# Kernel tuning notes

Hardware: AMD Instinct MI355X
Metric: run time of the kernel (lower is better)

The kernel has to match this reference:

```python
import jax, jax.numpy as jnp
import numpy as np

N_NODES = 50000
N_EDGES = 500000
D = 256  # node_dim = edge_dim = out_dim; in_dim = 2*D


def setup_inputs() -> dict:
    key = jax.random.key(0)
    ks = jax.random.split(key, 9)
    x = jax.random.normal(ks[0], (N_NODES, D), dtype=jnp.float32)
    edge_index = jax.random.randint(ks[1], (2, N_EDGES), 0, N_NODES, dtype=jnp.int64)
    edge_attr = jax.random.normal(ks[2], (N_EDGES, D), dtype=jnp.float32)
    u = jax.random.normal(ks[3], (1, D), dtype=jnp.float32)
    batch = jnp.zeros((N_NODES,), dtype=jnp.int64)
    scale = 1.0 / np.sqrt(2 * D)
    W1 = jax.random.normal(ks[4], (2 * D, D), dtype=jnp.float32) * scale
    b1 = jax.random.normal(ks[5], (D,), dtype=jnp.float32) * scale
    W2 = jax.random.normal(ks[6], (2 * D, D), dtype=jnp.float32) * scale
    b2 = jax.random.normal(ks[7], (D,), dtype=jnp.float32) * scale
    return {"x": x, "edge_index": edge_index, "edge_attr": edge_attr, "u": u,
            "batch": batch, "W1": W1, "b1": b1, "W2": W2, "b2": b2}


def reference(x, edge_index, edge_attr, u, batch, W1, b1, W2, b2):
    row, col = edge_index[0], edge_index[1]
    # gather source-node features and concat with edge features: [E, 2D]
    h = jnp.concatenate([x[row], edge_attr], axis=1)
    h = jax.nn.relu(h @ W1 + b1)  # node_mlp_1
    # scatter-mean over destination nodes
    agg = jax.ops.segment_sum(h, col, num_segments=N_NODES)
    cnt = jax.ops.segment_sum(jnp.ones((h.shape[0],), h.dtype), col, num_segments=N_NODES)
    agg = agg / jnp.maximum(cnt, 1.0)[:, None]
    out = jnp.concatenate([x, agg], axis=1)  # [N, 2D]
    return jax.nn.relu(out @ W2 + b2)  # node_mlp_2
```

## Files before the change

kernel.cpp:

```cpp
#include <hip/hip_runtime.h>

#define N_NODES 50000
#define N_EDGES 500000
#define D 256
#define TWO_D 512

typedef __attribute__((ext_vector_type(8))) __bf16 bf16x8;
typedef __attribute__((ext_vector_type(4))) float f32x4;
typedef unsigned short ushort_t;

__device__ __forceinline__ unsigned short f2bf(float f) {
    unsigned int u = __builtin_bit_cast(unsigned int, f);
    u += 0x7FFFu + ((u >> 16) & 1u);
    return (unsigned short)(u >> 16);
}
__device__ __forceinline__ unsigned int pk2(float lo, float hi) {
    return (unsigned int)f2bf(lo) | ((unsigned int)f2bf(hi) << 16);
}


__global__ void k_zero(float* __restrict__ p, int n4) {
    int i = blockIdx.x * blockDim.x + threadIdx.x;
    if (i < n4) ((float4*)p)[i] = make_float4(0.f, 0.f, 0.f, 0.f);
}

__global__ void k_cvt_x(const float* __restrict__ x, ushort_t* __restrict__ xb, int n8) {
    int i = blockIdx.x * blockDim.x + threadIdx.x;
    if (i < n8) {
        const float4* s = (const float4*)(x + (size_t)i * 8);
        float4 a = s[0], b = s[1];
        uint4 o;
        o.x = pk2(a.x, a.y); o.y = pk2(a.z, a.w);
        o.z = pk2(b.x, b.y); o.w = pk2(b.z, b.w);
        *(uint4*)(xb + (size_t)i * 8) = o;
    }
}

__global__ void k_wt(const float* __restrict__ w, ushort_t* __restrict__ wt, int KW) {
    int n = blockIdx.x;
    for (int k = threadIdx.x; k < KW; k += blockDim.x)
        wt[(size_t)n * KW + k] = f2bf(w[(size_t)k * D + n]);
}

__global__ void k_count_i(const int* __restrict__ coli, int* __restrict__ cnt) {
    int e = blockIdx.x * blockDim.x + threadIdx.x;
    if (e < N_EDGES) atomicAdd(&cnt[coli[e]], 1);
}


__device__ __forceinline__ int iscan_block(int v, int tid) {
    int lane = tid & 63, wv = tid >> 6;
    int s = v;
    #pragma unroll
    for (int off = 1; off < 64; off <<= 1) {
        int t = __shfl_up(s, off, 64);
        if (lane >= off) s += t;
    }
    __shared__ int wsum[4];
    if (lane == 63) wsum[wv] = s;
    __syncthreads();
    #pragma unroll
    for (int w = 0; w < 3; ++w)
        if (wv > w) s += wsum[w];
    return s;
}

__global__ void k_scan_a(const int* __restrict__ cnt, int* __restrict__ rowptr,
                         int* __restrict__ bsum) {
    int i = blockIdx.x * 256 + threadIdx.x;
    int v = (i < N_NODES) ? cnt[i] : 0;
    int s = iscan_block(v, threadIdx.x);
    if (i < N_NODES) rowptr[i] = s - v;
    if (threadIdx.x == 255) bsum[blockIdx.x] = s;
}

__global__ void k_scan_b(int* __restrict__ bsum, int nb) {
    int i = threadIdx.x;
    int v = (i < nb) ? bsum[i] : 0;
    int s = iscan_block(v, i);
    if (i < nb) bsum[i] = s - v;
}

__global__ void k_scan_c(int* __restrict__ rowptr, const int* __restrict__ bsum,
                         int* __restrict__ cursor) {
    int i = blockIdx.x * 256 + threadIdx.x;
    if (i < N_NODES) {
        int r = rowptr[i] + bsum[blockIdx.x];
        rowptr[i] = r;
        cursor[i] = r;
    }
    if (i == 0) rowptr[N_NODES] = N_EDGES;
}

__global__ void k_fill(const int* __restrict__ coli, const int* __restrict__ rowi,
                       int* __restrict__ cursor, int* __restrict__ elist,
                       int* __restrict__ rowg) {
    int e = blockIdx.x * blockDim.x + threadIdx.x;
    if (e < N_EDGES) {
        int p = atomicAdd(&cursor[coli[e]], 1);
        elist[p] = e;
        rowg[p] = rowi[e];
    }
}

__global__ void k_posnode(const int* __restrict__ rowptr, int* __restrict__ posnode) {
    int p = blockIdx.x * blockDim.x + threadIdx.x;
    if (p >= N_EDGES) return;
    int lo = 0, hi = N_NODES;
    while (hi - lo > 1) {
        int mid = (lo + hi) >> 1;
        if (rowptr[mid] <= p) lo = mid; else hi = mid;
    }
    posnode[p] = lo;
}

__global__ __launch_bounds__(256) void k_xw1(
    const ushort_t* __restrict__ xb, const ushort_t* __restrict__ w1at,
    const float* __restrict__ b1, float* __restrict__ xw1)
{
    __shared__ __align__(16) ushort_t As[64 * 64];
    __shared__ __align__(16) ushort_t Bs[256 * 64];
    const int tid = threadIdx.x;
    const int wave = tid >> 6, lane = tid & 63;
    const int lr = lane & 15, lh = lane >> 4;
    const int n0 = blockIdx.x * 64;

    const int sm = tid >> 2;
    const int sc = (tid & 3) << 4;
    int ns = n0 + sm; if (ns >= N_NODES) ns = N_NODES - 1;
    const ushort_t* xrow = xb + (size_t)ns * D;
    const ushort_t* wrow = w1at + (size_t)tid * D;
    const int swA = (sm & 7) << 3;
    const int swB = (tid & 7) << 3;

    f32x4 acc[4][4];
    #pragma unroll
    for (int i = 0; i < 4; ++i)
        #pragma unroll
        for (int j = 0; j < 4; ++j)
            acc[i][j] = (f32x4){0.f, 0.f, 0.f, 0.f};

    for (int kk = 0; kk < 4; ++kk) {
        const int k0 = kk << 6;
        const uint4* sx = (const uint4*)(xrow + k0 + sc);
        uint4 av0 = sx[0], av1 = sx[1];
        const uint4* wsv = (const uint4*)(wrow + k0);
        uint4 w0 = wsv[0], w1 = wsv[1], w2 = wsv[2], w3 = wsv[3];
        uint4 w4 = wsv[4], w5 = wsv[5], w6 = wsv[6], w7 = wsv[7];

        __syncthreads();
        *(uint4*)&As[sm * 64 + ( sc      ^ swA)] = av0;
        *(uint4*)&As[sm * 64 + ((sc + 8) ^ swA)] = av1;
        {
            const int base = tid * 64;
            *(uint4*)&Bs[base + ( 0 ^ swB)] = w0;
            *(uint4*)&Bs[base + ( 8 ^ swB)] = w1;
            *(uint4*)&Bs[base + (16 ^ swB)] = w2;
            *(uint4*)&Bs[base + (24 ^ swB)] = w3;
            *(uint4*)&Bs[base + (32 ^ swB)] = w4;
            *(uint4*)&Bs[base + (40 ^ swB)] = w5;
            *(uint4*)&Bs[base + (48 ^ swB)] = w6;
            *(uint4*)&Bs[base + (56 ^ swB)] = w7;
        }
        __syncthreads();

        #pragma unroll
        for (int kh = 0; kh < 2; ++kh) {
            const int kb = kh * 32 + lh * 8;
            bf16x8 af[4], bfr[4];
            #pragma unroll
            for (int i = 0; i < 4; ++i) {
                int m = i * 16 + lr;
                af[i] = *(const bf16x8*)&As[m * 64 + (kb ^ ((m & 7) << 3))];
            }
            #pragma unroll
            for (int j = 0; j < 4; ++j) {
                int n = wave * 64 + j * 16 + lr;
                bfr[j] = *(const bf16x8*)&Bs[n * 64 + (kb ^ ((n & 7) << 3))];
            }
            #pragma unroll
            for (int i = 0; i < 4; ++i)
                #pragma unroll
                for (int j = 0; j < 4; ++j)
                    acc[i][j] = __builtin_amdgcn_mfma_f32_16x16x32_bf16(af[i], bfr[j], acc[i][j], 0, 0, 0);
        }
    }

    float bv[4];
    #pragma unroll
    for (int j = 0; j < 4; ++j) bv[j] = b1[wave * 64 + j * 16 + lr];
    #pragma unroll
    for (int i = 0; i < 4; ++i) {
        #pragma unroll
        for (int r = 0; r < 4; ++r) {
            int m = i * 16 + lh * 4 + r;
            int node = n0 + m;
            if (node < N_NODES) {
                float* orow = xw1 + (size_t)node * D;
                #pragma unroll
                for (int j = 0; j < 4; ++j)
                    orow[wave * 64 + j * 16 + lr] = acc[i][j][r] + bv[j];
            }
        }
    }
}

__global__ __launch_bounds__(256, 3) void k_edge_csr(
    const float* __restrict__ ea, const ushort_t* __restrict__ w1bt,
    const float* __restrict__ xw1, const int* __restrict__ elist,
    const int* __restrict__ rowg, const int* __restrict__ posnode,
    const int* __restrict__ rowptr, float* __restrict__ agg)
{
    __shared__ __align__(16) ushort_t As[64 * 40];
    __shared__ __align__(16) ushort_t Bs[256 * 40];
    __shared__ int snd[64];
    const int tid = threadIdx.x;
    const int wave = tid >> 6, lane = tid & 63;
    const int lr = lane & 15, lh = lane >> 4;
    const int p0 = blockIdx.x * 64;

    if (tid < 64) {
        int p = p0 + tid;
        snd[tid] = (p < N_EDGES) ? posnode[min(p, N_EDGES - 1)] : -1;
    }

    const int sm = tid >> 2;
    const int scq = (tid & 3) << 3;
    int ps = p0 + sm; if (ps >= N_EDGES) ps = N_EDGES - 1;
    const int es = elist[ps];
    const float* earow = ea + (size_t)es * D;
    const ushort_t* wrow = w1bt + (size_t)tid * D;

    f32x4 acc[4][4];
    #pragma unroll
    for (int i = 0; i < 4; ++i)
        #pragma unroll
        for (int j = 0; j < 4; ++j)
            acc[i][j] = (f32x4){0.f, 0.f, 0.f, 0.f};

    #pragma unroll 1
    for (int kk = 0; kk < 8; ++kk) {
        const int k0 = kk << 5;
        const float4* s = (const float4*)(earow + k0 + scq);
        float4 f0 = s[0], f1 = s[1];
        uint4 av;
        av.x = pk2(f0.x, f0.y); av.y = pk2(f0.z, f0.w);
        av.z = pk2(f1.x, f1.y); av.w = pk2(f1.z, f1.w);
        const uint4* w = (const uint4*)(wrow + k0);
        uint4 w0 = w[0], w1 = w[1], w2 = w[2], w3 = w[3];

        __syncthreads();
        *(uint4*)&As[sm * 40 + scq] = av;
        {
            ushort_t* bb = &Bs[tid * 40];
            *(uint4*)&bb[ 0] = w0;
            *(uint4*)&bb[ 8] = w1;
            *(uint4*)&bb[16] = w2;
            *(uint4*)&bb[24] = w3;
        }
        __syncthreads();

        {
            const int kb = lh * 8;
            bf16x8 af[4], bfr[4];
            #pragma unroll
            for (int i = 0; i < 4; ++i)
                af[i] = *(const bf16x8*)&As[(i * 16 + lr) * 40 + kb];
            #pragma unroll
            for (int j = 0; j < 4; ++j)
                bfr[j] = *(const bf16x8*)&Bs[(wave * 64 + j * 16 + lr) * 40 + kb];
            #pragma unroll
            for (int i = 0; i < 4; ++i)
                #pragma unroll
                for (int j = 0; j < 4; ++j)
                    acc[i][j] = __builtin_amdgcn_mfma_f32_16x16x32_bf16(af[i], bfr[j], acc[i][j], 0, 0, 0);
        }
    }

    #pragma unroll
    for (int i = 0; i < 4; ++i) {
        #pragma unroll
        for (int r = 0; r < 4; ++r) {
            const int m = i * 16 + lh * 4 + r;
            const bool ok = (p0 + m < N_EDGES);
            const int srw = rowg[min(p0 + m, N_EDGES - 1)];
            const float* xr = xw1 + (size_t)srw * D + wave * 64 + lr;
            #pragma unroll
            for (int j = 0; j < 4; ++j) {
                float v = acc[i][j][r] + xr[j * 16];
                v = v > 0.f ? v : 0.f;
                acc[i][j][r] = ok ? v : 0.f;
            }
        }
    }

    int a = 0;
    while (a < 64) {
        const int node = snd[a];
        int b = a + 1;
        while (b < 64 && snd[b] == node) ++b;
        if (node >= 0) {
            float s0 = 0.f, s1 = 0.f, s2 = 0.f, s3 = 0.f;
            #pragma unroll
            for (int i = 0; i < 4; ++i) {
                if (b <= i * 16 || a >= (i + 1) * 16) continue;
                #pragma unroll
                for (int r = 0; r < 4; ++r) {
                    const int m = i * 16 + lh * 4 + r;
                    const bool in = (m >= a) && (m < b);
                    s0 += in ? acc[i][0][r] : 0.f;
                    s1 += in ? acc[i][1][r] : 0.f;
                    s2 += in ? acc[i][2][r] : 0.f;
                    s3 += in ? acc[i][3][r] : 0.f;
                }
            }
            s0 += __shfl_xor(s0, 16, 64); s0 += __shfl_xor(s0, 32, 64);
            s1 += __shfl_xor(s1, 16, 64); s1 += __shfl_xor(s1, 32, 64);
            s2 += __shfl_xor(s2, 16, 64); s2 += __shfl_xor(s2, 32, 64);
            s3 += __shfl_xor(s3, 16, 64); s3 += __shfl_xor(s3, 32, 64);
            if (lh == 0) {
                const bool interior = (rowptr[node] >= p0) && (rowptr[node + 1] <= p0 + 64);
                float* dst = agg + (size_t)node * D + wave * 64 + lr;
                if (interior) {
                    dst[0]  = s0; dst[16] = s1; dst[32] = s2; dst[48] = s3;
                } else {
                    atomicAdd(&dst[0],  s0); atomicAdd(&dst[16], s1);
                    atomicAdd(&dst[32], s2); atomicAdd(&dst[48], s3);
                }
            }
        }
        a = b;
    }
}

__global__ __launch_bounds__(256) void k_node(
    const ushort_t* __restrict__ xb, const float* __restrict__ agg,
    const int* __restrict__ cnti,
    const ushort_t* __restrict__ w2t, const float* __restrict__ b2,
    float* __restrict__ out)
{
    __shared__ __align__(16) ushort_t As[64 * 64];
    __shared__ __align__(16) ushort_t Bs[256 * 64];
    const int tid = threadIdx.x;
    const int wave = tid >> 6, lane = tid & 63;
    const int lr = lane & 15, lh = lane >> 4;
    const int n0 = blockIdx.x * 64;

    const int sm = tid >> 2;
    const int sc = (tid & 3) << 4;
    int ns = n0 + sm; if (ns >= N_NODES) ns = N_NODES - 1;
    const ushort_t* xrow = xb + (size_t)ns * D;
    const float*    arow = agg + (size_t)ns * D;
    const float     ic   = 1.0f / fmaxf((float)cnti[ns], 1.0f);
    const ushort_t* wrow = w2t + (size_t)tid * TWO_D;
    const int swA = (sm & 7) << 3;
    const int swB = (tid & 7) << 3;

    f32x4 acc[4][4];
    #pragma unroll
    for (int i = 0; i < 4; ++i)
        #pragma unroll
        for (int j = 0; j < 4; ++j)
            acc[i][j] = (f32x4){0.f, 0.f, 0.f, 0.f};

    for (int kk = 0; kk < 8; ++kk) {
        const int k0 = kk << 6;
        uint4 av0, av1;
        if (kk < 4) {
            const uint4* s = (const uint4*)(xrow + k0 + sc);
            av0 = s[0]; av1 = s[1];
        } else {
            const float4* s = (const float4*)(arow + (k0 - D) + sc);
            float4 f0 = s[0], f1 = s[1], f2 = s[2], f3 = s[3];
            f0.x *= ic; f0.y *= ic; f0.z *= ic; f0.w *= ic;
            f1.x *= ic; f1.y *= ic; f1.z *= ic; f1.w *= ic;
            f2.x *= ic; f2.y *= ic; f2.z *= ic; f2.w *= ic;
            f3.x *= ic; f3.y *= ic; f3.z *= ic; f3.w *= ic;
            av0.x = pk2(f0.x, f0.y); av0.y = pk2(f0.z, f0.w);
            av0.z = pk2(f1.x, f1.y); av0.w = pk2(f1.z, f1.w);
            av1.x = pk2(f2.x, f2.y); av1.y = pk2(f2.z, f2.w);
            av1.z = pk2(f3.x, f3.y); av1.w = pk2(f3.z, f3.w);
        }
        const uint4* wsv = (const uint4*)(wrow + k0);
        uint4 w0 = wsv[0], w1 = wsv[1], w2 = wsv[2], w3 = wsv[3];
        uint4 w4 = wsv[4], w5 = wsv[5], w6 = wsv[6], w7 = wsv[7];

        __syncthreads();
        *(uint4*)&As[sm * 64 + ( sc      ^ swA)] = av0;
        *(uint4*)&As[sm * 64 + ((sc + 8) ^ swA)] = av1;
        {
            const int base = tid * 64;
            *(uint4*)&Bs[base + ( 0 ^ swB)] = w0;
            *(uint4*)&Bs[base + ( 8 ^ swB)] = w1;
            *(uint4*)&Bs[base + (16 ^ swB)] = w2;
            *(uint4*)&Bs[base + (24 ^ swB)] = w3;
            *(uint4*)&Bs[base + (32 ^ swB)] = w4;
            *(uint4*)&Bs[base + (40 ^ swB)] = w5;
            *(uint4*)&Bs[base + (48 ^ swB)] = w6;
            *(uint4*)&Bs[base + (56 ^ swB)] = w7;
        }
        __syncthreads();

        #pragma unroll
        for (int kh = 0; kh < 2; ++kh) {
            const int kb = kh * 32 + lh * 8;
            bf16x8 af[4], bfr[4];
            #pragma unroll
            for (int i = 0; i < 4; ++i) {
                int m = i * 16 + lr;
                af[i] = *(const bf16x8*)&As[m * 64 + (kb ^ ((m & 7) << 3))];
            }
            #pragma unroll
            for (int j = 0; j < 4; ++j) {
                int n = wave * 64 + j * 16 + lr;
                bfr[j] = *(const bf16x8*)&Bs[n * 64 + (kb ^ ((n & 7) << 3))];
            }
            #pragma unroll
            for (int i = 0; i < 4; ++i)
                #pragma unroll
                for (int j = 0; j < 4; ++j)
                    acc[i][j] = __builtin_amdgcn_mfma_f32_16x16x32_bf16(af[i], bfr[j], acc[i][j], 0, 0, 0);
        }
    }

    float bv[4];
    #pragma unroll
    for (int j = 0; j < 4; ++j) bv[j] = b2[wave * 64 + j * 16 + lr];
    #pragma unroll
    for (int i = 0; i < 4; ++i) {
        #pragma unroll
        for (int r = 0; r < 4; ++r) {
            int m = i * 16 + lh * 4 + r;
            int node = n0 + m;
            if (node < N_NODES) {
                float* orow = out + (size_t)node * D;
                #pragma unroll
                for (int j = 0; j < 4; ++j) {
                    float v = acc[i][j][r] + bv[j];
                    orow[wave * 64 + j * 16 + lr] = v > 0.f ? v : 0.f;
                }
            }
        }
    }
}


extern "C" void kernel_launch(void* const* d_in, const int* in_sizes, int n_in,
                              void* d_out, int out_size, void* d_ws, size_t ws_size,
                              hipStream_t stream)
{
    const float* x  = (const float*)d_in[0];
    const int*   ei = (const int*)d_in[1];
    const float* ea = (const float*)d_in[2];
    const float* W1 = (const float*)d_in[5];
    const float* b1 = (const float*)d_in[6];
    const float* W2 = (const float*)d_in[7];
    const float* b2 = (const float*)d_in[8];
    float* out = (float*)d_out;

    const int* rowi = ei;
    const int* coli = ei + N_EDGES;
    char* ws = (char*)d_ws;

    size_t off = 0;
    auto take = [&](size_t bytes) {
        char* p = ws + off;
        off = (off + bytes + 255) & ~(size_t)255;
        return p;
    };

    ushort_t* xb      = (ushort_t*)take((size_t)N_NODES * D * 2);
    ushort_t* w1at    = (ushort_t*)take((size_t)D * D * 2);
    ushort_t* w1bt    = (ushort_t*)take((size_t)D * D * 2);
    ushort_t* w2t     = (ushort_t*)take((size_t)D * TWO_D * 2);
    float*    xw1     = (float*)take((size_t)N_NODES * D * 4);
    float*    agg     = (float*)take((size_t)N_NODES * D * 4);
    int*      cnti    = (int*)take(50016 * 4);
    int*      rowptr  = (int*)take(50016 * 4);
    int*      cursor  = (int*)take(50016 * 4);
    int*      bsum    = (int*)take(256 * 4);
    int*      elist   = (int*)take((size_t)N_EDGES * 4);
    int*      rowg    = (int*)take((size_t)N_EDGES * 4);
    int*      posnode = (int*)take((size_t)N_EDGES * 4);

    const int NB = (N_NODES + 255) / 256;
    const int EB = (N_EDGES + 255) / 256;
    const int NGB = (N_NODES + 63) / 64;
    const int EGB = (N_EDGES + 63) / 64;

    k_cvt_x<<<(N_NODES * D / 8 + 255) / 256, 256, 0, stream>>>(x, xb, N_NODES * D / 8);
    k_wt   <<<D, 256, 0, stream>>>(W1, w1at, D);
    k_wt   <<<D, 256, 0, stream>>>(W1 + (size_t)D * D, w1bt, D);
    k_wt   <<<D, 256, 0, stream>>>(W2, w2t, TWO_D);

    k_zero   <<<49, 256, 0, stream>>>((float*)cnti, 50016 / 4);
    k_count_i<<<EB, 256, 0, stream>>>(coli, cnti);
    k_scan_a <<<NB, 256, 0, stream>>>(cnti, rowptr, bsum);
    k_scan_b <<<1, 256, 0, stream>>>(bsum, NB);
    k_scan_c <<<NB, 256, 0, stream>>>(rowptr, bsum, cursor);
    k_fill   <<<EB, 256, 0, stream>>>(coli, rowi, cursor, elist, rowg);
    k_posnode<<<EB, 256, 0, stream>>>(rowptr, posnode);

    k_xw1    <<<NGB, 256, 0, stream>>>(xb, w1at, b1, xw1);
    k_zero   <<<(N_NODES * D / 4 + 255) / 256, 256, 0, stream>>>(agg, N_NODES * D / 4);
    k_edge_csr<<<EGB, 256, 0, stream>>>(ea, w1bt, xw1, elist, rowg, posnode, rowptr, agg);
    k_node   <<<NGB, 256, 0, stream>>>(xb, agg, cnti, w2t, b2, out);
}
```

Measured before the change: 502.4 us.

## Load MFMA operands directly from global memory, dropping LDS staging in edge kernel

The edge GEMM kernel no longer stages the edge-feature and weight tiles through shared memory with two barriers per K step. Each lane now loads its own A fragments (converted from fp32 to bf16) and B fragments straight from global memory into registers, and the K loop is unrolled by two. This removes the LDS traffic and the synchronisation, but each of the four waves now loads the full A tile separately, so A-side global and cache traffic is four times higher. The per-lane accesses are also less coalesced. A barrier is added before the segment reduction so the shared node-index array is ready.

```diff
diff --git a/kernel.cpp b/kernel.cpp
--- a/kernel.cpp
+++ b/kernel.cpp
@@ -211,8 +211,6 @@
     const int* __restrict__ rowg, const int* __restrict__ posnode,
     const int* __restrict__ rowptr, float* __restrict__ agg)
 {
-    __shared__ __align__(16) ushort_t As[64 * 40];
-    __shared__ __align__(16) ushort_t Bs[256 * 40];
     __shared__ int snd[64];
     const int tid = threadIdx.x;
     const int wave = tid >> 6, lane = tid & 63;
@@ -224,12 +222,16 @@
         snd[tid] = (p < N_EDGES) ? posnode[min(p, N_EDGES - 1)] : -1;
     }
 
-    const int sm = tid >> 2;
-    const int scq = (tid & 3) << 3;
-    int ps = p0 + sm; if (ps >= N_EDGES) ps = N_EDGES - 1;
-    const int es = elist[ps];
-    const float* earow = ea + (size_t)es * D;
-    const ushort_t* wrow = w1bt + (size_t)tid * D;
+    const float* pea[4];
+    #pragma unroll
+    for (int i = 0; i < 4; ++i) {
+        const int p = min(p0 + i * 16 + lr, N_EDGES - 1);
+        pea[i] = ea + (size_t)elist[p] * D + lh * 8;
+    }
+    const ushort_t* pw[4];
+    #pragma unroll
+    for (int j = 0; j < 4; ++j)
+        pw[j] = w1bt + (size_t)(wave * 64 + j * 16 + lr) * D + lh * 8;
 
     f32x4 acc[4][4];
     #pragma unroll
@@ -238,43 +240,27 @@
         for (int j = 0; j < 4; ++j)
             acc[i][j] = (f32x4){0.f, 0.f, 0.f, 0.f};
 
-    #pragma unroll 1
+    #pragma unroll 2
     for (int kk = 0; kk < 8; ++kk) {
         const int k0 = kk << 5;
-        const float4* s = (const float4*)(earow + k0 + scq);
-        float4 f0 = s[0], f1 = s[1];
-        uint4 av;
-        av.x = pk2(f0.x, f0.y); av.y = pk2(f0.z, f0.w);
-        av.z = pk2(f1.x, f1.y); av.w = pk2(f1.z, f1.w);
-        const uint4* w = (const uint4*)(wrow + k0);
-        uint4 w0 = w[0], w1 = w[1], w2 = w[2], w3 = w[3];
-
-        __syncthreads();
-        *(uint4*)&As[sm * 40 + scq] = av;
-        {
-            ushort_t* bb = &Bs[tid * 40];
-            *(uint4*)&bb[ 0] = w0;
-            *(uint4*)&bb[ 8] = w1;
-            *(uint4*)&bb[16] = w2;
-            *(uint4*)&bb[24] = w3;
-        }
-        __syncthreads();
-
-        {
-            const int kb = lh * 8;
-            bf16x8 af[4], bfr[4];
-            #pragma unroll
-            for (int i = 0; i < 4; ++i)
-                af[i] = *(const bf16x8*)&As[(i * 16 + lr) * 40 + kb];
+        bf16x8 af[4], bfr[4];
+        #pragma unroll
+        for (int i = 0; i < 4; ++i) {
+            const float4* s = (const float4*)(pea[i] + k0);
+            float4 f0 = s[0], f1 = s[1];
+            uint4 av;
+            av.x = pk2(f0.x, f0.y); av.y = pk2(f0.z, f0.w);
+            av.z = pk2(f1.x, f1.y); av.w = pk2(f1.z, f1.w);
+            af[i] = __builtin_bit_cast(bf16x8, av);
+        }
+        #pragma unroll
+        for (int j = 0; j < 4; ++j)
+            bfr[j] = *(const bf16x8*)(pw[j] + k0);
+        #pragma unroll
+        for (int i = 0; i < 4; ++i)
             #pragma unroll
             for (int j = 0; j < 4; ++j)
-                bfr[j] = *(const bf16x8*)&Bs[(wave * 64 + j * 16 + lr) * 40 + kb];
-            #pragma unroll
-            for (int i = 0; i < 4; ++i)
-                #pragma unroll
-                for (int j = 0; j < 4; ++j)
-                    acc[i][j] = __builtin_amdgcn_mfma_f32_16x16x32_bf16(af[i], bfr[j], acc[i][j], 0, 0, 0);
-        }
+                acc[i][j] = __builtin_amdgcn_mfma_f32_16x16x32_bf16(af[i], bfr[j], acc[i][j], 0, 0, 0);
     }
 
     #pragma unroll
@@ -293,6 +279,8 @@
             }
         }
     }
+
+    __syncthreads();
 
     int a = 0;
     while (a < 64) {
```

New measurement: 666.0 us. +32.6%, slower.
